# Optimization experiments

Hardware: AMD Instinct MI355X
Metric: run time of the kernel (lower is better)

Reference implementation:

```python
import jax, jax.numpy as jnp
import numpy as np

N = 262144
D = 512
H = 512
G = 1024


def setup_inputs() -> dict:
    key = jax.random.key(0)
    k1, k2, k3, k4 = jax.random.split(key, 4)
    embed = jax.random.normal(k1, (N, D), dtype=jnp.float32)
    batch_index = jnp.sort(jax.random.randint(k2, (N,), 0, G)).astype(jnp.int64)
    # nn.Linear weights: W_att [atten_hidden, embed_size], V_att [1, atten_hidden]
    W_att = jax.random.normal(k3, (H, D), dtype=jnp.float32) * (1.0 / np.sqrt(D))
    V_att = jax.random.normal(k4, (1, H), dtype=jnp.float32) * (1.0 / np.sqrt(H))
    return {"embed": embed, "batch_index": batch_index, "W_att": W_att, "V_att": V_att, "num_segments": G}


def reference(embed, batch_index, W_att, V_att, num_segments):
    # beta = V(tanh(W(embed))).squeeze(-1)  -> [N]
    beta = jnp.einsum('nh,oh->no', jnp.tanh(jnp.einsum('nd,hd->nh', embed, W_att)), V_att).squeeze(-1)
    # segment softmax (unnormalized exp, as in the original module)
    exp_beta = jnp.exp(beta)
    grouped_sum = jax.ops.segment_sum(exp_beta, batch_index, num_segments=num_segments)  # [G]
    alpha = exp_beta / grouped_sum[batch_index]  # [N]
    # scatter-weighted sum of node embeddings per graph -> [G, D]
    result = jax.ops.segment_sum(alpha[:, None] * embed, batch_index, num_segments=num_segments)
    return result
```

## Files before the change

kernel.cpp:

```cpp
#include <hip/hip_runtime.h>
#include <hip/hip_bf16.h>

#define D_DIM 512
#define H_DIM 512
#define G_SEG 1024
#define BM    128

typedef __attribute__((ext_vector_type(8))) short bf16x8;
typedef __attribute__((ext_vector_type(4))) float f32x4;
typedef unsigned int u32;
typedef unsigned short u16;

#define WS_S   0
#define WS_WB  8192

#define AS_BYTES  (128 * 1024)
#define BETA_OFF  AS_BYTES
#define EBS_OFF   (BETA_OFF + 4 * 128 * 4)
#define SIDX_OFF  (EBS_OFF + 128 * 4)
#define LDS_TOTAL (SIDX_OFF + 128 * 4)

static __device__ __forceinline__ u16 f2bf(float f) {
    __hip_bfloat16 h = __float2bfloat16(f);
    return *(u16*)&h;
}
static __device__ __forceinline__ float bf2f(u16 u) {
    return __uint_as_float(((u32)u) << 16);
}
static __device__ __forceinline__ float fast_tanh(float x) {
    float e = exp2f(x * 2.885390081777927f);
    return 1.0f - 2.0f * __builtin_amdgcn_rcpf(e + 1.0f);
}

__global__ __launch_bounds__(256)
void cvt_w(const float* __restrict__ W, u16* __restrict__ Wb) {
    int t   = blockIdx.x * 256 + threadIdx.x;
    int lhi = t & 3;
    int c   = (t >> 2) & 511;
    int k32 = t >> 11;
    const float* src = W + (size_t)c * 512 + k32 * 32 + lhi * 8;
    float4 f0 = *(const float4*)(src);
    float4 f1 = *(const float4*)(src + 4);
    u16 h[8];
    h[0]=f2bf(f0.x); h[1]=f2bf(f0.y); h[2]=f2bf(f0.z); h[3]=f2bf(f0.w);
    h[4]=f2bf(f1.x); h[5]=f2bf(f1.y); h[6]=f2bf(f1.z); h[7]=f2bf(f1.w);
    *(uint4*)(Wb + (size_t)t * 8) = *(uint4*)h;
}

__global__ __launch_bounds__(512, 2)
void fused(const float* __restrict__ E, const int* __restrict__ BI,
           const u16* __restrict__ Wb, const float* __restrict__ V,
           float* __restrict__ out, float* __restrict__ S)
{
    extern __shared__ char smem[];
    const int tid = threadIdx.x;
    const int nodeBase = blockIdx.x * BM;
    const int l   = tid & 63;
    const int w   = tid >> 6;
    const int wr  = w >> 2;
    const int wc  = w & 3;
    const int l15 = l & 15;
    const int lhi = l >> 4;

    const float* Eb = E + (size_t)nodeBase * 512;
    const int arow = tid >> 3;
    const int aj   = tid & 7;

    f32x4 acc[4][8];
#pragma unroll
    for (int m = 0; m < 4; ++m)
#pragma unroll
        for (int n = 0; n < 8; ++n) acc[m][n] = (f32x4){0.f, 0.f, 0.f, 0.f};

    float4 aload[4];
    {
        const float* p0 = Eb + (size_t)arow * 512 + aj * 8;
        aload[0] = *(const float4*)p0;       aload[1] = *(const float4*)(p0 + 4);
        const float* p1 = p0 + 64 * 512;
        aload[2] = *(const float4*)p1;       aload[3] = *(const float4*)(p1 + 4);
    }

    for (int ks = 0; ks < 8; ++ks) {
        {
            u16 h[8];
            h[0]=f2bf(aload[0].x); h[1]=f2bf(aload[0].y); h[2]=f2bf(aload[0].z); h[3]=f2bf(aload[0].w);
            h[4]=f2bf(aload[1].x); h[5]=f2bf(aload[1].y); h[6]=f2bf(aload[1].z); h[7]=f2bf(aload[1].w);
            int byte0 = arow * 1024 + ((ks * 128 + aj * 16) ^ ((arow & 7) << 4));
            *(uint4*)(smem + byte0) = *(uint4*)h;
            h[0]=f2bf(aload[2].x); h[1]=f2bf(aload[2].y); h[2]=f2bf(aload[2].z); h[3]=f2bf(aload[2].w);
            h[4]=f2bf(aload[3].x); h[5]=f2bf(aload[3].y); h[6]=f2bf(aload[3].z); h[7]=f2bf(aload[3].w);
            *(uint4*)(smem + byte0 + 64 * 1024) = *(uint4*)h;
        }
        if (ks < 7) {
            const float* p0 = Eb + (size_t)arow * 512 + (ks + 1) * 64 + aj * 8;
            aload[0] = *(const float4*)p0;   aload[1] = *(const float4*)(p0 + 4);
            const float* p1 = p0 + 64 * 512;
            aload[2] = *(const float4*)p1;   aload[3] = *(const float4*)(p1 + 4);
        }
        __syncthreads();

#pragma unroll
        for (int ksub = 0; ksub < 2; ++ksub) {
            const char* Wsub = (const char*)Wb + ((size_t)(ks * 2 + ksub) << 15);
            bf16x8 b[8];
#pragma unroll
            for (int n = 0; n < 8; ++n) {
                int c = wc * 128 + n * 16 + l15;
                b[n] = *(const bf16x8*)(Wsub + (c * 4 + lhi) * 16);
            }
            bf16x8 a[4];
            const int kbyte = ks * 128 + ksub * 64 + lhi * 16;
#pragma unroll
            for (int m = 0; m < 4; ++m) {
                int row = wr * 64 + m * 16 + l15;
                a[m] = *(const bf16x8*)(smem + row * 1024 + (kbyte ^ ((row & 7) << 4)));
            }
#pragma unroll
            for (int m = 0; m < 4; ++m)
#pragma unroll
                for (int n = 0; n < 8; ++n)
                    acc[m][n] = __builtin_amdgcn_mfma_f32_16x16x32_bf16(a[m], b[n], acc[m][n], 0, 0, 0);
        }
    }

    float Vv[8];
#pragma unroll
    for (int n = 0; n < 8; ++n)
        Vv[n] = V[wc * 128 + n * 16 + l15];

    float bsum[4][4];
#pragma unroll
    for (int m = 0; m < 4; ++m)
#pragma unroll
        for (int r = 0; r < 4; ++r) {
            float s = 0.f;
#pragma unroll
            for (int n = 0; n < 8; ++n)
                s += Vv[n] * fast_tanh(acc[m][n][r]);
            bsum[m][r] = s;
        }
#pragma unroll
    for (int off = 1; off <= 8; off <<= 1)
#pragma unroll
        for (int m = 0; m < 4; ++m)
#pragma unroll
            for (int r = 0; r < 4; ++r)
                bsum[m][r] += __shfl_xor(bsum[m][r], off, 64);

    float* betaP = (float*)(smem + BETA_OFF);
    if (l15 == 0) {
#pragma unroll
        for (int m = 0; m < 4; ++m)
#pragma unroll
            for (int r = 0; r < 4; ++r)
                betaP[wc * 128 + wr * 64 + m * 16 + lhi * 4 + r] = bsum[m][r];
    }
    __syncthreads();

    float* ebs  = (float*)(smem + EBS_OFF);
    int*   sidx = (int*)(smem + SIDX_OFF);
    if (tid < 128) {
        float beta = betaP[tid] + betaP[128 + tid] + betaP[256 + tid] + betaP[384 + tid];
        float eb = expf(beta);
        ebs[tid] = eb;
        int g = BI[nodeBase + tid];
        sidx[tid] = g;
        int g0 = __shfl(g, 0, 64);
        if (__all(g == g0)) {
            float s = eb;
#pragma unroll
            for (int off = 1; off <= 32; off <<= 1)
                s += __shfl_xor(s, off, 64);
            if (l == 0) atomicAdd(&S[g], s);
        } else {
            atomicAdd(&S[g], eb);
        }
    }
    __syncthreads();

    const int c = tid;
    float a = 0.f;
    int gcur = sidx[0];
    for (int r = 0; r < 128; ++r) {
        int g = sidx[r];
        if (g != gcur) {
            atomicAdd(&out[(size_t)gcur * 512 + c], a);
            a = 0.f; gcur = g;
        }
        u16 v = *(const u16*)(smem + r * 1024 + ((2 * c) ^ ((r & 7) << 4)));
        a += ebs[r] * bf2f(v);
    }
    atomicAdd(&out[(size_t)gcur * 512 + c], a);
}

__global__ __launch_bounds__(256)
void finalize_kernel(float* __restrict__ out, const float* __restrict__ S) {
    int idx = blockIdx.x * 256 + threadIdx.x;
    float s = S[idx >> 9];
    float v = out[idx];
    out[idx] = (s != 0.f) ? v * __builtin_amdgcn_rcpf(s) : 0.f;
}

extern "C" void kernel_launch(void* const* d_in, const int* in_sizes, int n_in,
                              void* d_out, int out_size, void* d_ws, size_t ws_size,
                              hipStream_t stream) {
    const float* E  = (const float*)d_in[0];
    const int*   BI = (const int*)d_in[1];
    const float* W  = (const float*)d_in[2];
    const float* V  = (const float*)d_in[3];
    float* out = (float*)d_out;
    char*  ws  = (char*)d_ws;
    const int Ntot = in_sizes[0] / D_DIM;

    float* S  = (float*)(ws + WS_S);
    u16*   Wb = (u16*)(ws + WS_WB);

    hipMemsetAsync(S, 0, G_SEG * 4, stream);
    hipMemsetAsync(out, 0, (size_t)out_size * 4, stream);
    hipFuncSetAttribute((const void*)fused,
                        hipFuncAttributeMaxDynamicSharedMemorySize, LDS_TOTAL);

    cvt_w<<<128, 256, 0, stream>>>(W, Wb);
    fused<<<Ntot / BM, 512, LDS_TOTAL, stream>>>(E, BI, Wb, V, out, S);
    finalize_kernel<<<out_size / 256, 256, 0, stream>>>(out, S);
}
```

Baseline: 371.1 us.

## Double-buffer W fragments in registers and vectorize segment-sum epilogue

The GEMM loop now prefetches the next half-K slice of bf16 W fragments into a second register set (bA/bB ping-pong) while MFMAs consume the current one, hiding global/L2 load latency for W. The weighted segment reduction is restructured so each thread reads 8 bf16 columns with one 16-byte LDS load over a 16-row slice instead of one column over all 128 rows. This cuts LDS instruction count and shortens the serial loop, but it multiplies global atomics by up to 8x because each row slice flushes its own partials. Extra registers for the second B buffer may also pressure occupancy at 512 threads with 2 blocks per CU.

```diff
diff --git a/kernel.cpp b/kernel.cpp
--- a/kernel.cpp
+++ b/kernel.cpp
@@ -72,12 +72,22 @@
 #pragma unroll
         for (int n = 0; n < 8; ++n) acc[m][n] = (f32x4){0.f, 0.f, 0.f, 0.f};
 
+    const int bOffBase = ((wc * 128 + l15) * 4 + lhi) * 16;
+
     float4 aload[4];
     {
         const float* p0 = Eb + (size_t)arow * 512 + aj * 8;
         aload[0] = *(const float4*)p0;       aload[1] = *(const float4*)(p0 + 4);
         const float* p1 = p0 + 64 * 512;
         aload[2] = *(const float4*)p1;       aload[3] = *(const float4*)(p1 + 4);
+    }
+
+    bf16x8 bA[8], bB[8];
+    {
+        const char* Wsub = (const char*)Wb;
+#pragma unroll
+        for (int n = 0; n < 8; ++n)
+            bA[n] = *(const bf16x8*)(Wsub + bOffBase + n * (16 * 4 * 16));
     }
 
     for (int ks = 0; ks < 8; ++ks) {
@@ -99,17 +109,14 @@
         }
         __syncthreads();
 
-#pragma unroll
-        for (int ksub = 0; ksub < 2; ++ksub) {
-            const char* Wsub = (const char*)Wb + ((size_t)(ks * 2 + ksub) << 15);
-            bf16x8 b[8];
-#pragma unroll
-            for (int n = 0; n < 8; ++n) {
-                int c = wc * 128 + n * 16 + l15;
-                b[n] = *(const bf16x8*)(Wsub + (c * 4 + lhi) * 16);
-            }
+        {
+            const char* Wnext = (const char*)Wb + ((size_t)(ks * 2 + 1) << 15);
+#pragma unroll
+            for (int n = 0; n < 8; ++n)
+                bB[n] = *(const bf16x8*)(Wnext + bOffBase + n * (16 * 4 * 16));
+
             bf16x8 a[4];
-            const int kbyte = ks * 128 + ksub * 64 + lhi * 16;
+            const int kbyte = ks * 128 + lhi * 16;
 #pragma unroll
             for (int m = 0; m < 4; ++m) {
                 int row = wr * 64 + m * 16 + l15;
@@ -119,7 +126,27 @@
             for (int m = 0; m < 4; ++m)
 #pragma unroll
                 for (int n = 0; n < 8; ++n)
-                    acc[m][n] = __builtin_amdgcn_mfma_f32_16x16x32_bf16(a[m], b[n], acc[m][n], 0, 0, 0);
+                    acc[m][n] = __builtin_amdgcn_mfma_f32_16x16x32_bf16(a[m], bA[n], acc[m][n], 0, 0, 0);
+        }
+        {
+            if (ks < 7) {
+                const char* Wnext = (const char*)Wb + ((size_t)(ks * 2 + 2) << 15);
+#pragma unroll
+                for (int n = 0; n < 8; ++n)
+                    bA[n] = *(const bf16x8*)(Wnext + bOffBase + n * (16 * 4 * 16));
+            }
+            bf16x8 a[4];
+            const int kbyte = ks * 128 + 64 + lhi * 16;
+#pragma unroll
+            for (int m = 0; m < 4; ++m) {
+                int row = wr * 64 + m * 16 + l15;
+                a[m] = *(const bf16x8*)(smem + row * 1024 + (kbyte ^ ((row & 7) << 4)));
+            }
+#pragma unroll
+            for (int m = 0; m < 4; ++m)
+#pragma unroll
+                for (int n = 0; n < 8; ++n)
+                    acc[m][n] = __builtin_amdgcn_mfma_f32_16x16x32_bf16(a[m], bB[n], acc[m][n], 0, 0, 0);
         }
     }
 
@@ -178,19 +205,35 @@
     }
     __syncthreads();
 
-    const int c = tid;
-    float a = 0.f;
-    int gcur = sidx[0];
-    for (int r = 0; r < 128; ++r) {
-        int g = sidx[r];
-        if (g != gcur) {
-            atomicAdd(&out[(size_t)gcur * 512 + c], a);
-            a = 0.f; gcur = g;
-        }
-        u16 v = *(const u16*)(smem + r * 1024 + ((2 * c) ^ ((r & 7) << 4)));
-        a += ebs[r] * bf2f(v);
-    }
-    atomicAdd(&out[(size_t)gcur * 512 + c], a);
+    {
+        const int c8    = tid & 63;
+        const int rbase = (tid >> 6) * 16;
+        const int cbyte = c8 * 16;
+        float a[8];
+#pragma unroll
+        for (int j = 0; j < 8; ++j) a[j] = 0.f;
+        int gcur = sidx[rbase];
+        for (int rr = 0; rr < 16; ++rr) {
+            int r = rbase + rr;
+            int g = sidx[r];
+            if (g != gcur) {
+                float* o = out + (size_t)gcur * 512 + c8 * 8;
+#pragma unroll
+                for (int j = 0; j < 8; ++j) atomicAdd(o + j, a[j]);
+#pragma unroll
+                for (int j = 0; j < 8; ++j) a[j] = 0.f;
+                gcur = g;
+            }
+            float wgt = ebs[r];
+            bf16x8 v = *(const bf16x8*)(smem + r * 1024 + (cbyte ^ ((r & 7) << 4)));
+#pragma unroll
+            for (int j = 0; j < 8; ++j)
+                a[j] += wgt * bf2f((u16)v[j]);
+        }
+        float* o = out + (size_t)gcur * 512 + c8 * 8;
+#pragma unroll
+        for (int j = 0; j < 8; ++j) atomicAdd(o + j, a[j]);
+    }
 }
 
 __global__ __launch_bounds__(256)
```

Result: slower. 531.7 us (+43.3%).

## Halve node tile to 64 and split H across all 8 waves

Applied to the files above, without the earlier changes.

Shrinks the per-block node tile from 128 to 64 rows and remaps the 8 waves so each owns a 64-column slice of H instead of a 2x4 wave grid, halving accumulators per wave and raising the occupancy target to 4 blocks per CU. The intent is more resident blocks and lower register and LDS pressure, giving better latency hiding on the streaming embed loads. In exchange, each W_att tile is reused across fewer rows, so total W traffic from cache doubles. Atomic flushes to out also rise because there are twice as many blocks. The ksub loop is no longer unrolled, which may reduce instruction-level overlap.

```diff
diff --git a/kernel.cpp b/kernel.cpp
--- a/kernel.cpp
+++ b/kernel.cpp
@@ -4,7 +4,7 @@
 #define D_DIM 512
 #define H_DIM 512
 #define G_SEG 1024
-#define BM    128
+#define BM    64
 
 typedef __attribute__((ext_vector_type(8))) short bf16x8;
 typedef __attribute__((ext_vector_type(4))) float f32x4;
@@ -14,11 +14,11 @@
 #define WS_S   0
 #define WS_WB  8192
 
-#define AS_BYTES  (128 * 1024)
+#define AS_BYTES  (BM * 1024)
 #define BETA_OFF  AS_BYTES
-#define EBS_OFF   (BETA_OFF + 4 * 128 * 4)
-#define SIDX_OFF  (EBS_OFF + 128 * 4)
-#define LDS_TOTAL (SIDX_OFF + 128 * 4)
+#define EBS_OFF   (BETA_OFF + 8 * BM * 4)
+#define SIDX_OFF  (EBS_OFF + BM * 4)
+#define LDS_TOTAL (SIDX_OFF + BM * 4)
 
 static __device__ __forceinline__ u16 f2bf(float f) {
     __hip_bfloat16 h = __float2bfloat16(f);
@@ -47,7 +47,7 @@
     *(uint4*)(Wb + (size_t)t * 8) = *(uint4*)h;
 }
 
-__global__ __launch_bounds__(512, 2)
+__global__ __launch_bounds__(512, 4)
 void fused(const float* __restrict__ E, const int* __restrict__ BI,
            const u16* __restrict__ Wb, const float* __restrict__ V,
            float* __restrict__ out, float* __restrict__ S)
@@ -57,8 +57,6 @@
     const int nodeBase = blockIdx.x * BM;
     const int l   = tid & 63;
     const int w   = tid >> 6;
-    const int wr  = w >> 2;
-    const int wc  = w & 3;
     const int l15 = l & 15;
     const int lhi = l >> 4;
 
@@ -66,18 +64,19 @@
     const int arow = tid >> 3;
     const int aj   = tid & 7;
 
-    f32x4 acc[4][8];
+    f32x4 acc[4][4];
 #pragma unroll
     for (int m = 0; m < 4; ++m)
 #pragma unroll
-        for (int n = 0; n < 8; ++n) acc[m][n] = (f32x4){0.f, 0.f, 0.f, 0.f};
-
-    float4 aload[4];
+        for (int n = 0; n < 4; ++n) acc[m][n] = (f32x4){0.f, 0.f, 0.f, 0.f};
+
+    const int bOffBase = ((w * 64 + l15) * 4 + lhi) * 16;
+
+    float4 aload[2];
     {
         const float* p0 = Eb + (size_t)arow * 512 + aj * 8;
-        aload[0] = *(const float4*)p0;       aload[1] = *(const float4*)(p0 + 4);
-        const float* p1 = p0 + 64 * 512;
-        aload[2] = *(const float4*)p1;       aload[3] = *(const float4*)(p1 + 4);
+        aload[0] = *(const float4*)p0;
+        aload[1] = *(const float4*)(p0 + 4);
     }
 
     for (int ks = 0; ks < 8; ++ks) {
@@ -87,46 +86,40 @@
             h[4]=f2bf(aload[1].x); h[5]=f2bf(aload[1].y); h[6]=f2bf(aload[1].z); h[7]=f2bf(aload[1].w);
             int byte0 = arow * 1024 + ((ks * 128 + aj * 16) ^ ((arow & 7) << 4));
             *(uint4*)(smem + byte0) = *(uint4*)h;
-            h[0]=f2bf(aload[2].x); h[1]=f2bf(aload[2].y); h[2]=f2bf(aload[2].z); h[3]=f2bf(aload[2].w);
-            h[4]=f2bf(aload[3].x); h[5]=f2bf(aload[3].y); h[6]=f2bf(aload[3].z); h[7]=f2bf(aload[3].w);
-            *(uint4*)(smem + byte0 + 64 * 1024) = *(uint4*)h;
         }
         if (ks < 7) {
             const float* p0 = Eb + (size_t)arow * 512 + (ks + 1) * 64 + aj * 8;
-            aload[0] = *(const float4*)p0;   aload[1] = *(const float4*)(p0 + 4);
-            const float* p1 = p0 + 64 * 512;
-            aload[2] = *(const float4*)p1;   aload[3] = *(const float4*)(p1 + 4);
+            aload[0] = *(const float4*)p0;
+            aload[1] = *(const float4*)(p0 + 4);
         }
         __syncthreads();
 
-#pragma unroll
+#pragma unroll 1
         for (int ksub = 0; ksub < 2; ++ksub) {
             const char* Wsub = (const char*)Wb + ((size_t)(ks * 2 + ksub) << 15);
-            bf16x8 b[8];
-#pragma unroll
-            for (int n = 0; n < 8; ++n) {
-                int c = wc * 128 + n * 16 + l15;
-                b[n] = *(const bf16x8*)(Wsub + (c * 4 + lhi) * 16);
-            }
+            bf16x8 b[4];
+#pragma unroll
+            for (int n = 0; n < 4; ++n)
+                b[n] = *(const bf16x8*)(Wsub + bOffBase + n * 1024);
             bf16x8 a[4];
             const int kbyte = ks * 128 + ksub * 64 + lhi * 16;
 #pragma unroll
             for (int m = 0; m < 4; ++m) {
-                int row = wr * 64 + m * 16 + l15;
+                int row = m * 16 + l15;
                 a[m] = *(const bf16x8*)(smem + row * 1024 + (kbyte ^ ((row & 7) << 4)));
             }
 #pragma unroll
             for (int m = 0; m < 4; ++m)
 #pragma unroll
-                for (int n = 0; n < 8; ++n)
+                for (int n = 0; n < 4; ++n)
                     acc[m][n] = __builtin_amdgcn_mfma_f32_16x16x32_bf16(a[m], b[n], acc[m][n], 0, 0, 0);
         }
     }
 
-    float Vv[8];
-#pragma unroll
-    for (int n = 0; n < 8; ++n)
-        Vv[n] = V[wc * 128 + n * 16 + l15];
+    float Vv[4];
+#pragma unroll
+    for (int n = 0; n < 4; ++n)
+        Vv[n] = V[w * 64 + n * 16 + l15];
 
     float bsum[4][4];
 #pragma unroll
@@ -135,7 +128,7 @@
         for (int r = 0; r < 4; ++r) {
             float s = 0.f;
 #pragma unroll
-            for (int n = 0; n < 8; ++n)
+            for (int n = 0; n < 4; ++n)
                 s += Vv[n] * fast_tanh(acc[m][n][r]);
             bsum[m][r] = s;
         }
@@ -153,14 +146,17 @@
         for (int m = 0; m < 4; ++m)
 #pragma unroll
             for (int r = 0; r < 4; ++r)
-                betaP[wc * 128 + wr * 64 + m * 16 + lhi * 4 + r] = bsum[m][r];
+                betaP[w * BM + m * 16 + lhi * 4 + r] = bsum[m][r];
     }
     __syncthreads();
 
     float* ebs  = (float*)(smem + EBS_OFF);
     int*   sidx = (int*)(smem + SIDX_OFF);
-    if (tid < 128) {
-        float beta = betaP[tid] + betaP[128 + tid] + betaP[256 + tid] + betaP[384 + tid];
+    if (tid < BM) {
+        float beta = 0.f;
+#pragma unroll
+        for (int j = 0; j < 8; ++j)
+            beta += betaP[j * BM + tid];
         float eb = expf(beta);
         ebs[tid] = eb;
         int g = BI[nodeBase + tid];
@@ -178,19 +174,21 @@
     }
     __syncthreads();
 
-    const int c = tid;
-    float a = 0.f;
-    int gcur = sidx[0];
-    for (int r = 0; r < 128; ++r) {
-        int g = sidx[r];
-        if (g != gcur) {
-            atomicAdd(&out[(size_t)gcur * 512 + c], a);
-            a = 0.f; gcur = g;
-        }
-        u16 v = *(const u16*)(smem + r * 1024 + ((2 * c) ^ ((r & 7) << 4)));
-        a += ebs[r] * bf2f(v);
-    }
-    atomicAdd(&out[(size_t)gcur * 512 + c], a);
+    {
+        const int c = tid;
+        float a = 0.f;
+        int gcur = sidx[0];
+        for (int r = 0; r < BM; ++r) {
+            int g = sidx[r];
+            if (g != gcur) {
+                atomicAdd(&out[(size_t)gcur * 512 + c], a);
+                a = 0.f; gcur = g;
+            }
+            u16 v = *(const u16*)(smem + r * 1024 + ((2 * c) ^ ((r & 7) << 4)));
+            a += ebs[r] * bf2f(v);
+        }
+        atomicAdd(&out[(size_t)gcur * 512 + c], a);
+    }
 }
 
 __global__ __launch_bounds__(256)
```

After: 333.4 us. 10.2% less time.
